# Performance work log

Hardware: AMD Instinct MI355X
Metric: run time of the kernel (lower is better)

## Reference

```python
import jax, jax.numpy as jnp
import numpy as np

B, T, I, H, C = 128, 512, 1024, 1024, 512


def setup_inputs() -> dict:
    key = jax.random.key(0)
    ks = jax.random.split(key, 10)
    s_i = 1.0 / np.sqrt(I)
    s_h = 1.0 / np.sqrt(H)
    s_c = 1.0 / np.sqrt(C)
    return {
        "x": jax.random.normal(ks[0], (B, T, I), jnp.float32),
        "h0": jax.random.normal(ks[1], (B, H), jnp.float32),
        "c0": jax.random.normal(ks[2], (B, H), jnp.float32),
        "ctx": jax.random.normal(ks[3], (B, C), jnp.float32),
        "Wi": jax.random.uniform(ks[4], (4 * H, I), jnp.float32, -s_i, s_i),
        "bi": jax.random.uniform(ks[5], (4 * H,), jnp.float32, -s_i, s_i),
        "Wh": jax.random.uniform(ks[6], (4 * H, H), jnp.float32, -s_h, s_h),
        "bh": jax.random.uniform(ks[7], (4 * H,), jnp.float32, -s_h, s_h),
        "Wc": jax.random.uniform(ks[8], (4 * H, C), jnp.float32, -s_c, s_c),
        "bc": jax.random.uniform(ks[9], (4 * H,), jnp.float32, -s_c, s_c),
    }


def reference(x, h0, c0, ctx, Wi, bi, Wh, bh, Wc, bc):
    # ctx contribution is constant across timesteps; fold it (and both biases)
    # into the precomputed per-step input gates. Math identical to per-step sum.
    ctx_g = ctx @ Wc.T + bc                              # [B,4H]
    xg = jnp.einsum('bti,gi->btg', x, Wi) + bi + ctx_g[:, None, :]  # [B,T,4H]
    xg = jnp.transpose(xg, (1, 0, 2))                    # [T,B,4H]

    def step(carry, g_t):
        h, c = carry
        gates = g_t + h @ Wh.T + bh                      # [B,4H]
        i_g, f_g, g_g, o_g = jnp.split(gates, 4, axis=1)
        i_g = jax.nn.sigmoid(i_g)
        f_g = jax.nn.sigmoid(f_g)
        g_g = jnp.tanh(g_g)
        o_g = jax.nn.sigmoid(o_g)
        c_new = f_g * c + i_g * g_g
        h_new = o_g * jnp.tanh(c_new)
        return (h_new, c_new), h_new

    (h_f, c_f), ys = jax.lax.scan(step, (h0, c0), xg)
    out = jnp.transpose(ys, (1, 0, 2))                   # [B,T,H] (batch_first)
    return out, h_f, c_f
```

## Files before the change

kernel.cpp:

```cpp
#include <hip/hip_runtime.h>
#include <hip/hip_bf16.h>


typedef __attribute__((ext_vector_type(8))) short short8;
typedef __attribute__((ext_vector_type(4))) float floatx4;
typedef unsigned short u16;
typedef unsigned int u32;

#define Bsz 128
#define Tsz 512
#define Isz 1024
#define Hsz 1024
#define G4  4096

__device__ __forceinline__ u16 f2bf(float f) {
    union { float f; u32 u; } v; v.f = f;
    u32 r = (v.u + 0x7fffu + ((v.u >> 16) & 1u)) >> 16;
    return (u16)r;
}
__device__ __forceinline__ float bf2f(u16 h) {
    union { u32 u; float f; } v; v.u = ((u32)h) << 16;
    return v.f;
}

__global__ void k_cast_w(const float* __restrict__ Wi, const float* __restrict__ Wh,
                         u16* __restrict__ WiB, u16* __restrict__ WhB) {
    int i = blockIdx.x * 256 + threadIdx.x;
    WiB[i] = f2bf(Wi[i]);
    WhB[i] = f2bf(Wh[i]);
}

__global__ void k_state(const float* __restrict__ h0, const float* __restrict__ c0,
                        u16* __restrict__ hbuf0, float* __restrict__ cws) {
    int i = blockIdx.x * 256 + threadIdx.x;
    hbuf0[i] = f2bf(h0[i]);
    cws[i] = c0[i];
}

__global__ void k_ctxg(const float* __restrict__ ctx, const float* __restrict__ Wc,
                       const float* __restrict__ bi, const float* __restrict__ bh,
                       const float* __restrict__ bc, float* __restrict__ ctxg) {
    int bid = blockIdx.x;
    int b = bid >> 4;
    int g = (bid & 15) * 256 + threadIdx.x;
    const float* wr = Wc + (long)g * 512;
    const float* cr = ctx + (long)b * 512;
    float s = 0.f;
    #pragma unroll 4
    for (int k = 0; k < 512; k += 4) {
        float4 w = *(const float4*)&wr[k];
        float4 c = *(const float4*)&cr[k];
        s += w.x * c.x + w.y * c.y + w.z * c.z + w.w * c.w;
    }
    ctxg[(long)b * G4 + g] = s + bi[g] + bh[g] + bc[g];
}

__global__ __launch_bounds__(256, 2)
void k_pre(const float* __restrict__ x, const u16* __restrict__ WiB,
           const float* __restrict__ ctxg, u16* __restrict__ pre) {
    const int bid = blockIdx.x;
    const int stripe = bid >> 5, nc = bid & 31;
    const long m0 = (long)stripe * 128;
    const int n0 = nc * 128;
    const int tid = threadIdx.x;
    const int lane = tid & 63, wid = tid >> 6;
    const int wm = wid >> 1, wn = wid & 1;

    __shared__ u16 As[128][72];
    __shared__ u16 Bs[128][72];

    floatx4 acc[4][4] = {};

    const int b = (int)(m0 >> 9);
    const int row = tid >> 1, half = tid & 1;
    const float* xsrc = x + (m0 + row) * Isz + half * 32;
    const u16*   wsrc = WiB + (long)(n0 + row) * Isz + half * 32;

    for (int kc = 0; kc < Isz; kc += 64) {
        const float4* xa = (const float4*)(xsrc + kc);
        #pragma unroll
        for (int j = 0; j < 8; j++) {
            float4 v = xa[j];
            u32 lo = (u32)f2bf(v.x) | ((u32)f2bf(v.y) << 16);
            u32 hi = (u32)f2bf(v.z) | ((u32)f2bf(v.w) << 16);
            *(uint2*)&As[row][half * 32 + j * 4] = make_uint2(lo, hi);
        }
        const uint4* wa = (const uint4*)(wsrc + kc);
        uint4* bdst = (uint4*)&Bs[row][half * 32];
        #pragma unroll
        for (int j = 0; j < 4; j++) bdst[j] = wa[j];
        __syncthreads();

        #pragma unroll
        for (int kk = 0; kk < 64; kk += 32) {
            const int qr = lane & 15;
            const int qk = kk + (lane >> 4) * 8;
            short8 af[4], bfr[4];
            #pragma unroll
            for (int i2 = 0; i2 < 4; i2++)
                af[i2] = *(const short8*)&As[wm * 64 + i2 * 16 + qr][qk];
            #pragma unroll
            for (int j2 = 0; j2 < 4; j2++)
                bfr[j2] = *(const short8*)&Bs[wn * 64 + j2 * 16 + qr][qk];
            #pragma unroll
            for (int i2 = 0; i2 < 4; i2++)
                #pragma unroll
                for (int j2 = 0; j2 < 4; j2++)
                    acc[i2][j2] = __builtin_amdgcn_mfma_f32_16x16x32_bf16(
                        af[i2], bfr[j2], acc[i2][j2], 0, 0, 0);
        }
        __syncthreads();
    }

    const int q4 = (lane >> 4) * 4, qc = lane & 15;
    #pragma unroll
    for (int i2 = 0; i2 < 4; i2++) {
        #pragma unroll
        for (int j2 = 0; j2 < 4; j2++) {
            const int gc = n0 + wn * 64 + j2 * 16 + qc;
            const float cv = ctxg[(long)b * G4 + gc];
            const long grow = m0 + wm * 64 + i2 * 16 + q4;
            #pragma unroll
            for (int r = 0; r < 4; r++)
                pre[(grow + r) * G4 + gc] = f2bf(acc[i2][j2][r] + cv);
        }
    }
}

__global__ __launch_bounds__(256)
void k_step(const u16* __restrict__ pre, const u16* __restrict__ WhB,
            const u16* __restrict__ hcur, u16* __restrict__ hnext,
            float* __restrict__ cws, float* __restrict__ out,
            float* __restrict__ hf, float* __restrict__ cf, int tt) {
    const int bid = blockIdx.x;
    const int mb = bid >> 6, nb = bid & 63;
    const int b0 = mb * 32, u0 = nb * 16;
    const int tid = threadIdx.x, lane = tid & 63, wid = tid >> 6;

    __shared__ u16 Hs[32][136];
    __shared__ u16 Ws[64][136];
    __shared__ float gbuf[4][32][16];

    floatx4 acc0 = {}, acc1 = {};

    const int hrow = tid >> 3, hoct = tid & 7;
    const int wrow = tid >> 2, wq = tid & 3;
    const int wgrp = wrow >> 4, wj = wrow & 15;
    const u16* hsrc = hcur + (long)(b0 + hrow) * Hsz + hoct * 16;
    const u16* wsrc = WhB + (long)(wgrp * Hsz + u0 + wj) * Hsz + wq * 32;

    for (int kc = 0; kc < Hsz; kc += 128) {
        const uint4* hs4 = (const uint4*)(hsrc + kc);
        uint4* hdst = (uint4*)&Hs[hrow][hoct * 16];
        hdst[0] = hs4[0]; hdst[1] = hs4[1];
        const uint4* ws4 = (const uint4*)(wsrc + kc);
        uint4* wdst = (uint4*)&Ws[wrow][wq * 32];
        #pragma unroll
        for (int j = 0; j < 4; j++) wdst[j] = ws4[j];
        __syncthreads();

        #pragma unroll
        for (int kk = 0; kk < 128; kk += 32) {
            const int qr = lane & 15;
            const int qk = kk + (lane >> 4) * 8;
            short8 a0 = *(const short8*)&Hs[qr][qk];
            short8 a1 = *(const short8*)&Hs[16 + qr][qk];
            short8 bfr = *(const short8*)&Ws[wid * 16 + qr][qk];
            acc0 = __builtin_amdgcn_mfma_f32_16x16x32_bf16(a0, bfr, acc0, 0, 0, 0);
            acc1 = __builtin_amdgcn_mfma_f32_16x16x32_bf16(a1, bfr, acc1, 0, 0, 0);
        }
        __syncthreads();
    }

    const int q4 = (lane >> 4) * 4, qc = lane & 15;
    #pragma unroll
    for (int mi = 0; mi < 2; mi++) {
        floatx4 a = mi ? acc1 : acc0;
        #pragma unroll
        for (int r = 0; r < 4; r++) {
            const int brow = mi * 16 + q4 + r;
            const long pidx = ((long)(b0 + brow) * Tsz + tt) * G4 + wid * Hsz + u0 + qc;
            float g = a[r] + bf2f(pre[pidx]);
            g = (wid == 2) ? tanhf(g) : 1.f / (1.f + __expf(-g));
            gbuf[wid][brow][qc] = g;
        }
    }
    __syncthreads();

    for (int e = tid; e < 512; e += 256) {
        const int brow = e >> 4, u = e & 15;
        const int bb = b0 + brow, un = u0 + u;
        const float ig = gbuf[0][brow][u];
        const float fg = gbuf[1][brow][u];
        const float gg = gbuf[2][brow][u];
        const float og = gbuf[3][brow][u];
        const long ci = (long)bb * Hsz + un;
        const float cn = fg * cws[ci] + ig * gg;
        const float hn = og * tanhf(cn);
        cws[ci] = cn;
        hnext[ci] = f2bf(hn);
        out[((long)bb * Tsz + tt) * Hsz + un] = hn;
        if (tt == 511) { hf[ci] = hn; cf[ci] = cn; }
    }
}

extern "C" void kernel_launch(void* const* d_in, const int* in_sizes, int n_in,
                              void* d_out, int out_size, void* d_ws, size_t ws_size,
                              hipStream_t stream) {
    const float* x   = (const float*)d_in[0];
    const float* h0  = (const float*)d_in[1];
    const float* c0  = (const float*)d_in[2];
    const float* ctx = (const float*)d_in[3];
    const float* Wi  = (const float*)d_in[4];
    const float* bi  = (const float*)d_in[5];
    const float* Wh  = (const float*)d_in[6];
    const float* bh  = (const float*)d_in[7];
    const float* Wc  = (const float*)d_in[8];
    const float* bc  = (const float*)d_in[9];

    float* out = (float*)d_out;
    float* hf  = out + (size_t)Bsz * Tsz * Hsz;
    float* cf  = hf + (size_t)Bsz * Hsz;

    char* ws = (char*)d_ws;
    u16*   pre  = (u16*)(ws);
    u16*   WiB  = (u16*)(ws + 536870912ull);
    u16*   WhB  = (u16*)(ws + 545259520ull);
    float* ctxg = (float*)(ws + 553648128ull);
    u16*   hbuf = (u16*)(ws + 555745280ull);
    float* cws  = (float*)(ws + 556269568ull);

    k_cast_w<<<16384, 256, 0, stream>>>(Wi, Wh, WiB, WhB);
    k_state<<<512, 256, 0, stream>>>(h0, c0, hbuf, cws);
    k_ctxg<<<2048, 256, 0, stream>>>(ctx, Wc, bi, bh, bc, ctxg);
    k_pre<<<16384, 256, 0, stream>>>(x, WiB, ctxg, pre);

    for (int tt = 0; tt < 512; tt++) {
        const u16* hc = hbuf + (size_t)(tt & 1) * (Bsz * Hsz);
        u16*       hn = hbuf + (size_t)((tt + 1) & 1) * (Bsz * Hsz);
        k_step<<<256, 256, 0, stream>>>(pre, WhB, hc, hn, cws, out, hf, cf, tt);
    }
}
```

Baseline: 9.271 ms.

## Replace per-step launches with persistent cooperative RNN kernel using register-resident weights

Replaces 512 separate per-timestep kernel launches with a single cooperative persistent kernel. Each of the 256 blocks keeps its slice of Wh in registers, keeps the cell state in registers, and synchronises per batch group through atomic counters in global memory. The precomputed gate tensor and the hidden state are re-laid out in tile-contiguous order, with swizzled LDS, so the per-step reads are coalesced. This removes launch overhead and the repeated Wh reloads each step. In exchange it relies on spin-wait barriers and all 256 blocks being co-resident.

```diff
diff --git a/kernel.cpp b/kernel.cpp
--- a/kernel.cpp
+++ b/kernel.cpp
@@ -1,5 +1,4 @@
 #include <hip/hip_runtime.h>
-#include <hip/hip_bf16.h>
 
 
 typedef __attribute__((ext_vector_type(8))) short short8;
@@ -23,6 +22,10 @@
     return v.f;
 }
 
+__device__ __forceinline__ int ht_off(int b, int u) {
+    return (((((b >> 4) * 32 + (u >> 5)) << 6) + (b & 15) + (((u >> 3) & 3) << 4)) << 3) + (u & 7);
+}
+
 __global__ void k_cast_w(const float* __restrict__ Wi, const float* __restrict__ Wh,
                          u16* __restrict__ WiB, u16* __restrict__ WhB) {
     int i = blockIdx.x * 256 + threadIdx.x;
@@ -30,11 +33,14 @@
     WhB[i] = f2bf(Wh[i]);
 }
 
-__global__ void k_state(const float* __restrict__ h0, const float* __restrict__ c0,
-                        u16* __restrict__ hbuf0, float* __restrict__ cws) {
+__global__ void k_state(const float* __restrict__ h0, u16* __restrict__ hT) {
     int i = blockIdx.x * 256 + threadIdx.x;
-    hbuf0[i] = f2bf(h0[i]);
-    cws[i] = c0[i];
+    int b = i >> 10, u = i & 1023;
+    hT[ht_off(b, u)] = f2bf(h0[i]);
+}
+
+__global__ void k_zero(u32* __restrict__ bar) {
+    bar[blockIdx.x * 256 + threadIdx.x] = 0;
 }
 
 __global__ void k_ctxg(const float* __restrict__ ctx, const float* __restrict__ Wc,
@@ -57,7 +63,7 @@
 
 __global__ __launch_bounds__(256, 2)
 void k_pre(const float* __restrict__ x, const u16* __restrict__ WiB,
-           const float* __restrict__ ctxg, u16* __restrict__ pre) {
+           const float* __restrict__ ctxg, u16* __restrict__ pre2) {
     const int bid = blockIdx.x;
     const int stripe = bid >> 5, nc = bid & 31;
     const long m0 = (long)stripe * 128;
@@ -113,94 +119,184 @@
     }
 
     const int q4 = (lane >> 4) * 4, qc = lane & 15;
+    const int g = n0 >> 10;
+    const int colb = g * 16 + qc;
+    const int mb2 = b >> 5, brow = b & 31;
+    const int nb_base = (n0 & 1023) >> 4;
     #pragma unroll
     for (int i2 = 0; i2 < 4; i2++) {
         #pragma unroll
         for (int j2 = 0; j2 < 4; j2++) {
             const int gc = n0 + wn * 64 + j2 * 16 + qc;
             const float cv = ctxg[(long)b * G4 + gc];
+            const int nbb = nb_base + wn * 4 + j2;
             const long grow = m0 + wm * 64 + i2 * 16 + q4;
             #pragma unroll
-            for (int r = 0; r < 4; r++)
-                pre[(grow + r) * G4 + gc] = f2bf(acc[i2][j2][r] + cv);
-        }
-    }
-}
-
-__global__ __launch_bounds__(256)
-void k_step(const u16* __restrict__ pre, const u16* __restrict__ WhB,
-            const u16* __restrict__ hcur, u16* __restrict__ hnext,
-            float* __restrict__ cws, float* __restrict__ out,
-            float* __restrict__ hf, float* __restrict__ cf, int tt) {
+            for (int r = 0; r < 4; r++) {
+                const int tt = (int)((grow + r) & 511);
+                pre2[(((long)tt * 4 + mb2) * 64 + nbb) * 2048 + brow * 64 + colb] =
+                    f2bf(acc[i2][j2][r] + cv);
+            }
+        }
+    }
+}
+
+__global__ __launch_bounds__(256, 1)
+void k_rnn(const u16* __restrict__ pre2, const u16* __restrict__ WhB,
+           u16* __restrict__ hT, const float* __restrict__ c0,
+           float* __restrict__ out, float* __restrict__ hf,
+           float* __restrict__ cf, u32* __restrict__ bar) {
     const int bid = blockIdx.x;
     const int mb = bid >> 6, nb = bid & 63;
     const int b0 = mb * 32, u0 = nb * 16;
-    const int tid = threadIdx.x, lane = tid & 63, wid = tid >> 6;
-
-    __shared__ u16 Hs[32][136];
-    __shared__ u16 Ws[64][136];
-    __shared__ float gbuf[4][32][16];
-
-    floatx4 acc0 = {}, acc1 = {};
-
-    const int hrow = tid >> 3, hoct = tid & 7;
-    const int wrow = tid >> 2, wq = tid & 3;
-    const int wgrp = wrow >> 4, wj = wrow & 15;
-    const u16* hsrc = hcur + (long)(b0 + hrow) * Hsz + hoct * 16;
-    const u16* wsrc = WhB + (long)(wgrp * Hsz + u0 + wj) * Hsz + wq * 32;
-
-    for (int kc = 0; kc < Hsz; kc += 128) {
-        const uint4* hs4 = (const uint4*)(hsrc + kc);
-        uint4* hdst = (uint4*)&Hs[hrow][hoct * 16];
-        hdst[0] = hs4[0]; hdst[1] = hs4[1];
-        const uint4* ws4 = (const uint4*)(wsrc + kc);
-        uint4* wdst = (uint4*)&Ws[wrow][wq * 32];
-        #pragma unroll
-        for (int j = 0; j < 4; j++) wdst[j] = ws4[j];
-        __syncthreads();
-
-        #pragma unroll
-        for (int kk = 0; kk < 128; kk += 32) {
-            const int qr = lane & 15;
-            const int qk = kk + (lane >> 4) * 8;
-            short8 a0 = *(const short8*)&Hs[qr][qk];
-            short8 a1 = *(const short8*)&Hs[16 + qr][qk];
-            short8 bfr = *(const short8*)&Ws[wid * 16 + qr][qk];
-            acc0 = __builtin_amdgcn_mfma_f32_16x16x32_bf16(a0, bfr, acc0, 0, 0, 0);
-            acc1 = __builtin_amdgcn_mfma_f32_16x16x32_bf16(a1, bfr, acc1, 0, 0, 0);
-        }
-        __syncthreads();
-    }
-
-    const int q4 = (lane >> 4) * 4, qc = lane & 15;
-    #pragma unroll
-    for (int mi = 0; mi < 2; mi++) {
-        floatx4 a = mi ? acc1 : acc0;
-        #pragma unroll
-        for (int r = 0; r < 4; r++) {
-            const int brow = mi * 16 + q4 + r;
-            const long pidx = ((long)(b0 + brow) * Tsz + tt) * G4 + wid * Hsz + u0 + qc;
-            float g = a[r] + bf2f(pre[pidx]);
-            g = (wid == 2) ? tanhf(g) : 1.f / (1.f + __expf(-g));
-            gbuf[wid][brow][qc] = g;
-        }
-    }
-    __syncthreads();
-
-    for (int e = tid; e < 512; e += 256) {
-        const int brow = e >> 4, u = e & 15;
-        const int bb = b0 + brow, un = u0 + u;
-        const float ig = gbuf[0][brow][u];
-        const float fg = gbuf[1][brow][u];
-        const float gg = gbuf[2][brow][u];
-        const float og = gbuf[3][brow][u];
-        const long ci = (long)bb * Hsz + un;
-        const float cn = fg * cws[ci] + ig * gg;
-        const float hn = og * tanhf(cn);
-        cws[ci] = cn;
-        hnext[ci] = f2bf(hn);
-        out[((long)bb * Tsz + tt) * Hsz + un] = hn;
-        if (tt == 511) { hf[ci] = hn; cf[ci] = cn; }
+    const int tid = threadIdx.x;
+    const int lane = tid & 63, kw = tid >> 6;
+
+    __shared__ float gpart[4][2048];
+    __shared__ float gact[2048];
+
+    short8 breg[4][8];
+    {
+        const int r16 = lane & 15;
+        const int k8 = (lane >> 4) * 8;
+        #pragma unroll
+        for (int g = 0; g < 4; g++) {
+            const long rowbase = (long)(g * Hsz + u0 + r16) * Hsz;
+            #pragma unroll
+            for (int ks = 0; ks < 8; ks++)
+                breg[g][ks] = *(const short8*)&WhB[rowbase + kw * 256 + ks * 32 + k8];
+        }
+    }
+
+    const int cu = tid & 15, cb = tid >> 4;
+    float creg0 = c0[(long)(b0 + cb) * Hsz + u0 + cu];
+    float creg1 = c0[(long)(b0 + cb + 16) * Hsz + u0 + cu];
+
+    const int rcol = tid & 63;
+    const int rrow0 = (tid >> 6) * 8;
+    const int rswz = (rcol & 7) << 2;
+
+    const int baseA0 = (((mb * 2) * 32 + kw * 8) * 64 + lane) * 8;
+    const int baseA1 = baseA0 + 32 * 64 * 8;
+
+    const int qc = lane & 15, q4 = (lane >> 4) * 4;
+
+    for (int t = 0; t < Tsz; t++) {
+        if (t > 0) {
+            if (tid == 0) {
+                const int bi2 = ((t - 1) * 4 + mb) << 4;
+                while (__hip_atomic_load(&bar[bi2], __ATOMIC_RELAXED,
+                                         __HIP_MEMORY_SCOPE_AGENT) < 64u)
+                    __builtin_amdgcn_s_sleep(2);
+                __threadfence();
+            }
+            __syncthreads();
+        }
+
+        const u16* hsrc = hT + (size_t)(t & 1) * 131072;
+
+        const u16* pbase = pre2 + (((long)t * 4 + mb) * 64 + nb) * 2048;
+        u16 pv[8];
+        #pragma unroll
+        for (int r = 0; r < 8; r++) pv[r] = pbase[(rrow0 + r) * 64 + rcol];
+
+        floatx4 acc[2][4];
+        #pragma unroll
+        for (int mi = 0; mi < 2; mi++)
+            #pragma unroll
+            for (int nj = 0; nj < 4; nj++)
+                acc[mi][nj] = (floatx4){0.f, 0.f, 0.f, 0.f};
+
+        #pragma unroll
+        for (int ks = 0; ks < 8; ks++) {
+            short8 a0 = *(const short8*)&hsrc[baseA0 + ks * 512];
+            short8 a1 = *(const short8*)&hsrc[baseA1 + ks * 512];
+            #pragma unroll
+            for (int nj = 0; nj < 4; nj++) {
+                acc[0][nj] = __builtin_amdgcn_mfma_f32_16x16x32_bf16(
+                    a0, breg[nj][ks], acc[0][nj], 0, 0, 0);
+                acc[1][nj] = __builtin_amdgcn_mfma_f32_16x16x32_bf16(
+                    a1, breg[nj][ks], acc[1][nj], 0, 0, 0);
+            }
+        }
+
+        #pragma unroll
+        for (int mi = 0; mi < 2; mi++)
+            #pragma unroll
+            for (int nj = 0; nj < 4; nj++) {
+                const int col = nj * 16 + qc;
+                const int e = (col * 32 + mi * 16 + q4) ^ ((col & 7) << 2);
+                *(floatx4*)&gpart[kw][e] = acc[mi][nj];
+            }
+        __syncthreads();
+
+        {
+            float gs[8];
+            #pragma unroll
+            for (int rr = 0; rr < 8; rr++) gs[rr] = bf2f(pv[rr]);
+            #pragma unroll
+            for (int p = 0; p < 4; p++) {
+                const int e0 = (rcol * 32 + rrow0) ^ rswz;
+                const int e1 = (rcol * 32 + rrow0 + 4) ^ rswz;
+                floatx4 v0 = *(const floatx4*)&gpart[p][e0];
+                floatx4 v1 = *(const floatx4*)&gpart[p][e1];
+                gs[0] += v0[0]; gs[1] += v0[1]; gs[2] += v0[2]; gs[3] += v0[3];
+                gs[4] += v1[0]; gs[5] += v1[1]; gs[6] += v1[2]; gs[7] += v1[3];
+            }
+            if ((rcol >> 4) == 2) {
+                #pragma unroll
+                for (int rr = 0; rr < 8; rr++) gs[rr] = tanhf(gs[rr]);
+            } else {
+                #pragma unroll
+                for (int rr = 0; rr < 8; rr++) gs[rr] = 1.f / (1.f + __expf(-gs[rr]));
+            }
+            floatx4 w0 = {gs[0], gs[1], gs[2], gs[3]};
+            floatx4 w1 = {gs[4], gs[5], gs[6], gs[7]};
+            *(floatx4*)&gact[(rcol * 32 + rrow0) ^ rswz] = w0;
+            *(floatx4*)&gact[(rcol * 32 + rrow0 + 4) ^ rswz] = w1;
+        }
+        __syncthreads();
+
+        {
+            const int swu = (cu & 7) << 2;
+            const int cbase = cu * 32;
+            const int gb0 = cb ^ swu;
+            const int gb1 = (cb + 16) ^ swu;
+            const float ig0 = gact[cbase + gb0];
+            const float fg0 = gact[512 + cbase + gb0];
+            const float gg0 = gact[1024 + cbase + gb0];
+            const float og0 = gact[1536 + cbase + gb0];
+            const float ig1 = gact[cbase + gb1];
+            const float fg1 = gact[512 + cbase + gb1];
+            const float gg1 = gact[1024 + cbase + gb1];
+            const float og1 = gact[1536 + cbase + gb1];
+
+            creg0 = fg0 * creg0 + ig0 * gg0;
+            creg1 = fg1 * creg1 + ig1 * gg1;
+            const float h0v = og0 * tanhf(creg0);
+            const float h1v = og1 * tanhf(creg1);
+
+            __builtin_nontemporal_store(h0v, &out[((long)(b0 + cb) * Tsz + t) * Hsz + u0 + cu]);
+            __builtin_nontemporal_store(h1v, &out[((long)(b0 + cb + 16) * Tsz + t) * Hsz + u0 + cu]);
+
+            u16* hdst = hT + (size_t)((t + 1) & 1) * 131072;
+            hdst[ht_off(b0 + cb, u0 + cu)] = f2bf(h0v);
+            hdst[ht_off(b0 + cb + 16, u0 + cu)] = f2bf(h1v);
+
+            if (t == Tsz - 1) {
+                hf[(long)(b0 + cb) * Hsz + u0 + cu] = h0v;
+                hf[(long)(b0 + cb + 16) * Hsz + u0 + cu] = h1v;
+                cf[(long)(b0 + cb) * Hsz + u0 + cu] = creg0;
+                cf[(long)(b0 + cb + 16) * Hsz + u0 + cu] = creg1;
+            }
+        }
+        __syncthreads();
+
+        if (tid == 0) {
+            __threadfence();
+            __hip_atomic_fetch_add(&bar[(t * 4 + mb) << 4], 1u,
+                                   __ATOMIC_RELEASE, __HIP_MEMORY_SCOPE_AGENT);
+        }
     }
 }
 
@@ -223,21 +319,23 @@
     float* cf  = hf + (size_t)Bsz * Hsz;
 
     char* ws = (char*)d_ws;
-    u16*   pre  = (u16*)(ws);
+    u16*   pre2 = (u16*)(ws);
     u16*   WiB  = (u16*)(ws + 536870912ull);
     u16*   WhB  = (u16*)(ws + 545259520ull);
     float* ctxg = (float*)(ws + 553648128ull);
-    u16*   hbuf = (u16*)(ws + 555745280ull);
-    float* cws  = (float*)(ws + 556269568ull);
+    u16*   hT   = (u16*)(ws + 555745280ull);
+    u32*   bar  = (u32*)(ws + 556269568ull);
 
     k_cast_w<<<16384, 256, 0, stream>>>(Wi, Wh, WiB, WhB);
-    k_state<<<512, 256, 0, stream>>>(h0, c0, hbuf, cws);
+    k_state<<<512, 256, 0, stream>>>(h0, hT);
     k_ctxg<<<2048, 256, 0, stream>>>(ctx, Wc, bi, bh, bc, ctxg);
-    k_pre<<<16384, 256, 0, stream>>>(x, WiB, ctxg, pre);
-
-    for (int tt = 0; tt < 512; tt++) {
-        const u16* hc = hbuf + (size_t)(tt & 1) * (Bsz * Hsz);
-        u16*       hn = hbuf + (size_t)((tt + 1) & 1) * (Bsz * Hsz);
-        k_step<<<256, 256, 0, stream>>>(pre, WhB, hc, hn, cws, out, hf, cf, tt);
-    }
-}
+    k_zero<<<128, 256, 0, stream>>>(bar);
+    k_pre<<<16384, 256, 0, stream>>>(x, WiB, ctxg, pre2);
+
+    const u16* pre2c = pre2;
+    const u16* WhBc  = WhB;
+    const float* c0c = c0;
+    void* args[] = {(void*)&pre2c, (void*)&WhBc, (void*)&hT, (void*)&c0c,
+                    (void*)&out, (void*)&hf, (void*)&cf, (void*)&bar};
+    hipLaunchCooperativeKernel((void*)k_rnn, dim3(256), dim3(256), args, 0, stream);
+}
```

After: 13.82 ms. 49.1% more time.
